# Kernel tuning notes

Hardware: AMD Instinct MI355X
Metric: run time of the kernel (lower is better)

Reference implementation:

```python
import jax, jax.numpy as jnp
from jax import lax
import numpy as np

N = 4
ALPHA_AP = 0.85
ALPHA_DS = 0.1
ALPHA_LR = 1.0
C1 = 0.01 ** 2
C2 = 0.03 ** 2


def resize_ac(img, nh, nw):
    # bilinear resize, align_corners=True (matches F.interpolate(..., align_corners=True))
    B, C, H, W = img.shape
    ys = jnp.linspace(0.0, H - 1.0, nh)
    xs = jnp.linspace(0.0, W - 1.0, nw)
    y0 = jnp.floor(ys).astype(jnp.int32)
    y1 = jnp.minimum(y0 + 1, H - 1)
    x0 = jnp.floor(xs).astype(jnp.int32)
    x1 = jnp.minimum(x0 + 1, W - 1)
    wy = (ys - y0).astype(img.dtype)[None, None, :, None]
    wx = (xs - x0).astype(img.dtype)[None, None, None, :]
    top = img[:, :, y0, :] * (1.0 - wy) + img[:, :, y1, :] * wy
    return top[:, :, :, x0] * (1.0 - wx) + top[:, :, :, x1] * wx


def build_pyramid(img):
    B, C, H, W = img.shape
    pyr = [img]
    for i in range(N - 1):
        r = 2 ** (i + 1)
        pyr.append(resize_ac(pyr[i], H // r, W // r))  # resize previous level, as in torch code
    return pyr


def x_grad(img):
    # replicate-pad right then diff -> last column is exactly zero
    g = img[:, :, :, :-1] - img[:, :, :, 1:]
    return jnp.concatenate([g, jnp.zeros_like(img[:, :, :, :1])], axis=3)


def y_grad(img):
    g = img[:, :, :-1, :] - img[:, :, 1:, :]
    return jnp.concatenate([g, jnp.zeros_like(img[:, :, :1, :])], axis=2)


def avgpool3(x):
    # AvgPool2d(3, 1), VALID padding
    return lax.reduce_window(x, 0.0, lax.add, (1, 1, 3, 3), (1, 1, 1, 1), 'VALID') / 9.0


def grid_sample_zeros(img, gx, gy):
    # bilinear grid_sample, padding_mode='zeros', align_corners=True
    B, C, H, W = img.shape
    x = (gx + 1.0) * 0.5 * (W - 1)
    y = (gy + 1.0) * 0.5 * (H - 1)
    x0 = jnp.floor(x)
    y0 = jnp.floor(y)

    def corner(xi, yi, w):
        valid = (xi >= 0) & (xi <= W - 1) & (yi >= 0) & (yi <= H - 1)
        xc = jnp.clip(xi, 0, W - 1).astype(jnp.int32)
        yc = jnp.clip(yi, 0, H - 1).astype(jnp.int32)
        vals = jax.vmap(lambda im, yy, xx: im[:, yy, xx])(img, yc, xc)  # [B,C,H,W]
        return vals * (w * valid.astype(img.dtype))[:, None]

    return (corner(x0, y0, (x0 + 1 - x) * (y0 + 1 - y))
            + corner(x0 + 1, y0, (x - x0) * (y0 + 1 - y))
            + corner(x0, y0 + 1, (x0 + 1 - x) * (y - y0))
            + corner(x0 + 1, y0 + 1, (x - x0) * (y - y0)))


def apply_disparity(img, disp):
    # standard Monodepth bilinear sampler: shift x_base in [0,1] by disp, grid_sample
    B, C, H, W = img.shape
    x_base = jnp.linspace(0.0, 1.0, W)[None, None, :]
    y_base = jnp.linspace(0.0, 1.0, H)[None, :, None]
    gx = 2.0 * (x_base + disp[:, 0]) - 1.0  # [B,H,W]
    gy = jnp.broadcast_to(2.0 * y_base - 1.0, gx.shape)
    return grid_sample_zeros(img, gx, gy)


def dssim(x, y):
    mu_x = avgpool3(x)
    mu_y = avgpool3(y)
    sig_x = avgpool3(x * x) - mu_x ** 2
    sig_y = avgpool3(y * y) - mu_y ** 2
    cov = avgpool3(x * y) - mu_x * mu_y
    ssim = ((2.0 * mu_x * mu_y + C1) * (2.0 * cov + C2)) / ((mu_x ** 2 + mu_y ** 2 + C1) * (sig_x + sig_y + C2))
    return jnp.mean(jnp.clip((1.0 - ssim) / 2.0, 0.0, 1.0))


def smoothness(disp, img, level):
    wx = jnp.exp(-jnp.mean(jnp.abs(x_grad(img)), axis=1, keepdims=True))
    wy = jnp.exp(-jnp.mean(jnp.abs(y_grad(img)), axis=1, keepdims=True))
    sx = x_grad(disp) * wx
    sy = y_grad(disp) * wy
    return jnp.mean(jnp.abs(sx) + jnp.abs(sy)) / (2 ** level)


def loss_forward(disps, left, right):
    lp = build_pyramid(left)
    rp = build_pyramid(right)
    dl = [d[:, 0:1] for d in disps]
    dr = [d[:, 1:2] for d in disps]
    left_est = [apply_disparity(rp[i], -dl[i]) for i in range(N)]
    right_est = [apply_disparity(lp[i], dr[i]) for i in range(N)]
    r2l_disp = [apply_disparity(dr[i], -dl[i]) for i in range(N)]
    l2r_disp = [apply_disparity(dl[i], dr[i]) for i in range(N)]
    # appearance matching (note: outer *ALPHA_AP matches the original's AP_loss*self.alpha_AP)
    AP = sum(ALPHA_AP * dssim(lp[i], left_est[i]) + (1.0 - ALPHA_AP) * jnp.mean(jnp.abs(lp[i] - left_est[i])) for i in range(N))
    AP = AP + sum(ALPHA_AP * dssim(rp[i], right_est[i]) + (1.0 - ALPHA_AP) * jnp.mean(jnp.abs(rp[i] - right_est[i])) for i in range(N))
    AP = AP * ALPHA_AP
    LR = sum(jnp.mean(jnp.abs(dl[i] - r2l_disp[i])) for i in range(N))
    LR = (LR + sum(jnp.mean(jnp.abs(dr[i] - l2r_disp[i])) for i in range(N))) * ALPHA_LR
    DS = sum(smoothness(dl[i], lp[i], i) for i in range(N))
    DS = (DS + sum(smoothness(dr[i], rp[i], i) for i in range(N))) * ALPHA_DS
    total = AP + LR + DS
    return total, AP, LR, DS


def setup_inputs() -> dict:
    key = jax.random.key(0)
    ks = jax.random.split(key, 6)
    B, H, W = 32, 256, 512
    inp = {}
    for i in range(N):
        h, w = H >> i, W >> i
        # normalized disparities in [0, 0.05) as in trained Monodepth
        inp[f'disp{i}'] = jax.random.uniform(ks[i], (B, 2, h, w), jnp.float32) * 0.05
    inp['left'] = jax.random.uniform(ks[4], (B, 3, H, W), jnp.float32)
    inp['right'] = jax.random.uniform(ks[5], (B, 3, H, W), jnp.float32)
    return inp


def reference(disp0, disp1, disp2, disp3, left, right):
    return loss_forward([disp0, disp1, disp2, disp3], left, right)
```

## Files before the change

### kernel.cpp

```cpp
#include <hip/hip_runtime.h>

#define BDIM 256
#define SH 16

typedef float v2f __attribute__((ext_vector_type(2)));

struct LevelDesc {
    const float* lp; const float* rp; const float* dp;
    int H, W, nCW, nRS, nPerSide, waveBase;
};
struct AllParams { LevelDesc lv[4]; int totalWaves; };

__device__ __forceinline__ float dpp_shl1(float x) {
    int r = __builtin_amdgcn_update_dpp(0, __float_as_int(x), 0x130, 0xF, 0xF, true);
    return __int_as_float(r);
}

__device__ __forceinline__ const float* uptr(const float* p) {
    unsigned long long u = (unsigned long long)p;
    unsigned lo = __builtin_amdgcn_readfirstlane((unsigned)u);
    unsigned hi = __builtin_amdgcn_readfirstlane((unsigned)(u >> 32));
    return (const float*)(((unsigned long long)hi << 32) | (unsigned long long)lo);
}

__device__ __forceinline__ v2f mkv(float a, float b) { v2f r; r.x = a; r.y = b; return r; }


__global__ void resize2_kernel(const float* __restrict__ sL, const float* __restrict__ sR,
                               float* __restrict__ dL, float* __restrict__ dR,
                               int BC, int Hs, int Ws, int Hd, int Wd,
                               double* acc, int doZero) {
    if (doZero && blockIdx.x == 0 && threadIdx.x < 33) acc[threadIdx.x] = 0.0;
    long long half = (long long)BC * Hd * Wd;
    long long idx = (long long)blockIdx.x * blockDim.x + threadIdx.x;
    if (idx >= 2 * half) return;
    const float* src = (idx < half) ? sL : sR;
    float* dst = (idx < half) ? dL : dR;
    long long id = (idx < half) ? idx : idx - half;
    int i = (int)(id % Wd);
    long long t = id / Wd;
    int j = (int)(t % Hd);
    int bc = (int)(t / Hd);
    float stepy = (float)(Hs - 1) / (float)(Hd - 1);
    float stepx = (float)(Ws - 1) / (float)(Wd - 1);
    float y = j * stepy;
    float x = i * stepx;
    int y0 = (int)floorf(y);
    int y1 = min(y0 + 1, Hs - 1);
    int x0 = (int)floorf(x);
    int x1 = min(x0 + 1, Ws - 1);
    float wy = y - (float)y0;
    float wx = x - (float)x0;
    const float* s = src + (long long)bc * Hs * Ws;
    float t0 = s[(long long)y0 * Ws + x0] * (1.0f - wy) + s[(long long)y1 * Ws + x0] * wy;
    float t1 = s[(long long)y0 * Ws + x1] * (1.0f - wy) + s[(long long)y1 * Ws + x1] * wy;
    dst[id] = t0 * (1.0f - wx) + t1 * wx;
}

#define S2Y (127.0f / 63.0f)
#define S2X (255.0f / 127.0f)
#define S3Y (63.0f / 31.0f)
#define S3X (127.0f / 63.0f)

__device__ __forceinline__ float bilA(const float* __restrict__ s, int j, int i) {
    float y = j * S2Y, x = i * S2X;
    int y0 = (int)floorf(y); int y1 = min(y0 + 1, 127);
    int x0 = (int)floorf(x); int x1 = min(x0 + 1, 255);
    float wy = y - (float)y0, wx = x - (float)x0;
    float t0 = s[y0 * 256 + x0] * (1.0f - wy) + s[y1 * 256 + x0] * wy;
    float t1 = s[y0 * 256 + x1] * (1.0f - wy) + s[y1 * 256 + x1] * wy;
    return t0 * (1.0f - wx) + t1 * wx;
}
__device__ __forceinline__ float bilB(const float* __restrict__ s, int j, int i) {
    float y = j * S3Y, x = i * S3X;
    int y0 = (int)floorf(y); int y1 = min(y0 + 1, 63);
    int x0 = (int)floorf(x); int x1 = min(x0 + 1, 127);
    float wy = y - (float)y0, wx = x - (float)x0;
    float v00 = bilA(s, y0, x0), v10 = bilA(s, y1, x0);
    float v01 = bilA(s, y0, x1), v11 = bilA(s, y1, x1);
    float t0 = v00 * (1.0f - wy) + v10 * wy;
    float t1 = v01 * (1.0f - wy) + v11 * wy;
    return t0 * (1.0f - wx) + t1 * wx;
}

__global__ void __launch_bounds__(256)
resize23_kernel(const float* __restrict__ l1, const float* __restrict__ r1,
                float* __restrict__ l2, float* __restrict__ r2,
                float* __restrict__ l3, float* __restrict__ r3) {
    const int n2 = 96 * 64 * 128;
    const int n3 = 96 * 32 * 64;
    int idx = blockIdx.x * 256 + threadIdx.x;
    if (idx < 2 * n2) {
        const float* src = (idx < n2) ? l1 : r1;
        float* dst = (idx < n2) ? l2 : r2;
        int id = (idx < n2) ? idx : idx - n2;
        int i = id & 127, j = (id >> 7) & 63, bc = id >> 13;
        dst[id] = bilA(src + bc * 32768, j, i);
    } else if (idx < 2 * n2 + 2 * n3) {
        int t = idx - 2 * n2;
        const float* src = (t < n3) ? l1 : r1;
        float* dst = (t < n3) ? l3 : r3;
        int id = (t < n3) ? t : t - n3;
        int i = id & 63, j = (id >> 6) & 31, bc = id >> 11;
        dst[id] = bilB(src + bc * 32768, j, i);
    }
}

__device__ __forceinline__ v2f ssim_term2(v2f Sx, v2f Sy, v2f Sxx, v2f Syy, v2f Sxy) {
    const float C1v = 0.0001f;
    const float C2v = 0.0009f;
    const float i9 = 1.0f / 9.0f;
    v2f mux = Sx * i9, muy = Sy * i9;
    v2f sigx = Sxx * i9 - mux * mux;
    v2f sigy = Syy * i9 - muy * muy;
    v2f cov  = Sxy * i9 - mux * muy;
    v2f num = ((2.0f * mux) * muy + C1v) * (2.0f * cov + C2v);
    v2f den = (mux * mux + muy * muy + C1v) * (sigx + sigy + C2v);
    v2f r;
    r.x = __builtin_amdgcn_rcpf(den.x);
    r.y = __builtin_amdgcn_rcpf(den.y);
    v2f v = (1.0f - num * r) * 0.5f;
    v2f o;
    o.x = __builtin_amdgcn_fmed3f(v.x, 0.0f, 1.0f);
    o.y = __builtin_amdgcn_fmed3f(v.y, 0.0f, 1.0f);
    return o;
}

struct RowVals {
    float d0, d1;
    v2f xv[3];
    v2f wI, wJ;
    v2f dI, dJ;
    v2f sI[3], sJ[3];
};

__global__ void __launch_bounds__(BDIM)
mega_kernel(AllParams P, double* __restrict__ acc, float* __restrict__ out) {
    const int lane = threadIdx.x & 63;
    const int wid  = threadIdx.x >> 6;
    const int wId  = blockIdx.x * (BDIM / 64) + wid;
    const int w = min(wId, P.totalWaves - 1);

    int level = 0;
    if (w >= P.lv[1].waveBase) level = 1;
    if (w >= P.lv[2].waveBase) level = 2;
    if (w >= P.lv[3].waveBase) level = 3;
    LevelDesc L;
    if (level == 0) L = P.lv[0];
    else if (level == 1) L = P.lv[1];
    else if (level == 2) L = P.lv[2];
    else L = P.lv[3];

    int rel = w - L.waveBase;
    const int side = (rel >= L.nPerSide) ? 1 : 0;
    rel -= side * L.nPerSide;
    const int cw = rel % L.nCW; rel /= L.nCW;
    const int rs = rel % L.nRS;
    const int b  = rel / L.nRS;

    const int H = L.H, W = L.W;
    const long long HW = (long long)H * W;
    const unsigned HWu = (unsigned)HW;
    const float Wm1f = (float)(W - 1);
    const float sgn = side ? 1.0f : -1.0f;

    const float* xim = uptr((side ? L.rp : L.lp) + (long long)b * 3 * HW);
    const float* sim = uptr((side ? L.lp : L.rp) + (long long)b * 3 * HW);
    const float* dme = uptr(L.dp + (long long)b * 2 * HW + (side ? HW : 0));
    const float* dot = uptr(L.dp + (long long)b * 2 * HW + (side ? 0 : HW));

    const int base = cw * 126;
    const int c0 = base + 2 * lane;
    const int c1 = c0 + 1;
    const bool in0 = c0 < W, in1 = c1 < W;
    const int cc = min(c0, W - 2) >> 1;
    const float fc0 = (float)c0, fc1 = (float)c1;

    const bool lastW = (cw == L.nCW - 1);
    const bool own0 = in0 && (c0 < base + 126 || lastW);
    const bool own1 = in1 && (c1 < base + 126 || lastW);
    const bool ownS0 = own0 && (c0 <= W - 3);
    const bool ownS1 = own1 && (c1 <= W - 3);

    const float mO0 = own0 ? 1.f : 0.f, mO1 = own1 ? 1.f : 0.f;
    const float mS0 = ownS0 ? 1.f : 0.f, mS1 = ownS1 ? 1.f : 0.f;
    const float mX0 = (own0 && c0 < W - 1) ? 1.f : 0.f;
    const float mX1 = (own1 && c1 < W - 1) ? 1.f : 0.f;

    const int r0 = rs * SH;
    const int r1 = min(r0 + SH, H);
    const int jend = min(r1 + 1, H - 1);

    v2f Pst[3][5], Lst[3][5];
#pragma unroll
    for (int c = 0; c < 3; ++c)
#pragma unroll
        for (int s = 0; s < 5; ++s) { Pst[c][s] = mkv(0.f, 0.f); Lst[c][s] = mkv(0.f, 0.f); }
    float pd0 = 0.f, pd1 = 0.f;
    v2f pxv[3] = {mkv(0.f,0.f), mkv(0.f,0.f), mkv(0.f,0.f)};

    float f_ss = 0.f, f_l1 = 0.f, f_lr = 0.f, f_ds = 0.f;

    auto load_dp = [&](int jj, float& o0, float& o1) {
        float2 dpair = ((const float2*)(dme + (unsigned)jj * (unsigned)W))[cc];
        o0 = dpair.x; o1 = dpair.y;
    };

    auto issue_gathers = [&](float di0, float di1, int jj, RowVals& R) {
        const unsigned ro = (unsigned)jj * (unsigned)W;
        R.d0 = di0; R.d1 = di1;
        float xq0 = fmaf(sgn * di0, Wm1f, fc0);
        float xq1 = fmaf(sgn * di1, Wm1f, fc1);
        float xf0 = floorf(xq0), xf1 = floorf(xq1);
        int g0 = (int)xf0, g1 = (int)xf1;
        float t0 = xq0 - xf0, t1 = xq1 - xf1;
        float w00 = (in0 && g0 >= 0 && g0 < W)         ? 1.0f - t0 : 0.0f;
        float w01 = (in0 && g0 >= -1 && g0 < W - 1)    ? t0        : 0.0f;
        float w10 = (in1 && g1 >= 0 && g1 < W)         ? 1.0f - t1 : 0.0f;
        float w11 = (in1 && g1 >= -1 && g1 < W - 1)    ? t1        : 0.0f;
        R.wI = mkv(w00, w10);
        R.wJ = mkv(w01, w11);
        unsigned a0 = ro + (unsigned)min(max(g0, 0), W - 1);
        unsigned a1 = ro + (unsigned)min(max(g0 + 1, 0), W - 1);
        unsigned b0 = ro + (unsigned)min(max(g1, 0), W - 1);
        unsigned b1 = ro + (unsigned)min(max(g1 + 1, 0), W - 1);
        R.dI = mkv(dot[a0], dot[b0]);
        R.dJ = mkv(dot[a1], dot[b1]);
#pragma unroll
        for (int c = 0; c < 3; ++c) {
            const unsigned co = (unsigned)c * HWu;
            float2 xp2 = ((const float2*)(xim + co + ro))[cc];
            R.xv[c] = mkv(in0 ? xp2.x : 0.f, in1 ? xp2.y : 0.f);
            R.sI[c] = mkv(sim[co + a0], sim[co + b0]);
            R.sJ[c] = mkv(sim[co + a1], sim[co + b1]);
        }
    };

    auto consume = [&](const RowVals& R, int j) {
        const float d0 = R.d0, d1 = R.d1;
        v2f wv2 = R.dI * R.wI + R.dJ * R.wJ;
        v2f xv[3], yv[3];
#pragma unroll
        for (int c = 0; c < 3; ++c) {
            xv[c] = R.xv[c];
            yv[c] = R.sI[c] * R.wI + R.sJ[c] * R.wJ;
        }

        const bool rowOwn = j < r1;
        if (rowOwn) {
            float s0 = fabsf(xv[0].x - yv[0].x) + fabsf(xv[1].x - yv[1].x) + fabsf(xv[2].x - yv[2].x);
            float s1 = fabsf(xv[0].y - yv[0].y) + fabsf(xv[1].y - yv[1].y) + fabsf(xv[2].y - yv[2].y);
            f_l1 = fmaf(mO0, s0, f_l1);
            f_l1 = fmaf(mO1, s1, f_l1);
            f_lr = fmaf(mO0, fabsf(d0 - wv2.x), f_lr);
            f_lr = fmaf(mO1, fabsf(d1 - wv2.y), f_lr);
        }

        {
            float dn  = dpp_shl1(d0);
            float xn0 = dpp_shl1(xv[0].x);
            float xn1 = dpp_shl1(xv[1].x);
            float xn2 = dpp_shl1(xv[2].x);
            if (rowOwn) {
                float g0v = fabsf(xv[0].x - xv[0].y) + fabsf(xv[1].x - xv[1].y) + fabsf(xv[2].x - xv[2].y);
                float g1v = fabsf(xv[0].y - xn0) + fabsf(xv[1].y - xn1) + fabsf(xv[2].y - xn2);
                f_ds = fmaf(mX0, fabsf((d0 - d1) * __expf(-g0v * (1.0f / 3.0f))), f_ds);
                f_ds = fmaf(mX1, fabsf((d1 - dn) * __expf(-g1v * (1.0f / 3.0f))), f_ds);
            }
        }
        if (j > r0 && (j - 1) < r1) {
            v2f t0 = pxv[0] - xv[0];
            v2f t1 = pxv[1] - xv[1];
            v2f t2 = pxv[2] - xv[2];
            float g0v = fabsf(t0.x) + fabsf(t1.x) + fabsf(t2.x);
            float g1v = fabsf(t0.y) + fabsf(t1.y) + fabsf(t2.y);
            f_ds = fmaf(mO0, fabsf((pd0 - d0) * __expf(-g0v * (1.0f / 3.0f))), f_ds);
            f_ds = fmaf(mO1, fabsf((pd1 - d1) * __expf(-g1v * (1.0f / 3.0f))), f_ds);
        }
        pd0 = d0; pd1 = d1;
#pragma unroll
        for (int c = 0; c < 3; ++c) pxv[c] = xv[c];

        const bool emit = (j >= r0 + 2);
#pragma unroll
        for (int c = 0; c < 3; ++c) {
            v2f X = xv[c], Y = yv[c];
            v2f V[5];
            V[0] = X; V[1] = Y;
            V[2] = X * X; V[3] = Y * Y; V[4] = X * Y;
            v2f cs[5];
#pragma unroll
            for (int s = 0; s < 5; ++s) {
                cs[s] = Pst[c][s] + V[s];
                Pst[c][s] = Lst[c][s] + V[s];
                Lst[c][s] = V[s];
            }
            if (emit) {
                v2f Wn[5];
#pragma unroll
                for (int s = 0; s < 5; ++s) {
                    float s0 = cs[s].x + cs[s].y;
                    Wn[s].x = s0 + dpp_shl1(cs[s].x);
                    Wn[s].y = cs[s].y + dpp_shl1(s0);
                }
                v2f ts = ssim_term2(Wn[0], Wn[1], Wn[2], Wn[3], Wn[4]);
                f_ss = fmaf(mS0, ts.x, f_ss);
                f_ss = fmaf(mS1, ts.y, f_ss);
            }
        }
    };

    RowVals A, B;
    float dq0, dq1, dn0, dn1;
    load_dp(r0, dq0, dq1);
    load_dp(min(r0 + 1, jend), dn0, dn1);
    issue_gathers(dq0, dq1, r0, A);

    int j = r0;
    for (;;) {
        float dp20, dp21;
        load_dp(min(j + 2, jend), dp20, dp21);
        if (j < jend) issue_gathers(dn0, dn1, j + 1, B);
        consume(A, j);
        dn0 = dp20; dn1 = dp21;
        if (++j > jend) break;

        load_dp(min(j + 2, jend), dp20, dp21);
        if (j < jend) issue_gathers(dn0, dn1, j + 1, A);
        consume(B, j);
        dn0 = dp20; dn1 = dp21;
        if (++j > jend) break;
    }

#pragma unroll
    for (int o = 32; o > 0; o >>= 1) {
        f_ss += __shfl_down(f_ss, o);
        f_l1 += __shfl_down(f_l1, o);
        f_lr += __shfl_down(f_lr, o);
        f_ds += __shfl_down(f_ds, o);
    }
    __shared__ float red[BDIM / 64][4];
    __shared__ int meta[2];
    if (threadIdx.x == 0) { meta[0] = level; meta[1] = side; }
    if (lane == 0) {
        red[wid][0] = f_ss; red[wid][1] = f_l1;
        red[wid][2] = f_lr; red[wid][3] = f_ds;
    }
    __syncthreads();
    if (threadIdx.x < 4) {
        int t = threadIdx.x;
        double s = (double)red[0][t] + (double)red[1][t]
                 + (double)red[2][t] + (double)red[3][t];
        atomicAdd(acc + t * 8 + meta[1] * 4 + meta[0], s);
    }

    if (threadIdx.x == 0) {
        asm volatile("s_waitcnt vmcnt(0)" ::: "memory");
        unsigned old = atomicAdd((unsigned*)(acc + 32), 1u);
        if (old == (unsigned)(gridDim.x - 1)) {
            const int B_ = 32, H0 = 256, W0 = 512;
            double AP = 0.0, LR = 0.0, DS = 0.0;
            for (int i = 0; i < 4; ++i) {
                int h = H0 >> i, ww = W0 >> i;
                double nss = (double)B_ * 3.0 * (double)(h - 2) * (double)(ww - 2);
                double nl1 = (double)B_ * 3.0 * (double)h * (double)ww;
                double nd  = (double)B_ * (double)h * (double)ww;
                double a0  = atomicAdd(acc + 0  + i, 0.0);
                double a4  = atomicAdd(acc + 4  + i, 0.0);
                double a8  = atomicAdd(acc + 8  + i, 0.0);
                double a12 = atomicAdd(acc + 12 + i, 0.0);
                double a16 = atomicAdd(acc + 16 + i, 0.0);
                double a20 = atomicAdd(acc + 20 + i, 0.0);
                double a24 = atomicAdd(acc + 24 + i, 0.0);
                double a28 = atomicAdd(acc + 28 + i, 0.0);
                AP += 0.85 * (a0 / nss) + 0.15 * (a8 / nl1);
                AP += 0.85 * (a4 / nss) + 0.15 * (a12 / nl1);
                LR += a16 / nd + a20 / nd;
                double sc = 1.0 / (double)(1 << i);
                DS += (a24 / nd) * sc + (a28 / nd) * sc;
            }
            AP *= 0.85;
            DS *= 0.1;
            double total = AP + LR + DS;
            out[0] = (float)total;
            out[1] = (float)AP;
            out[2] = (float)LR;
            out[3] = (float)DS;
        }
    }
}

extern "C" void kernel_launch(void* const* d_in, const int* in_sizes, int n_in,
                              void* d_out, int out_size, void* d_ws, size_t ws_size,
                              hipStream_t stream) {
    const int B = 32, H0 = 256, W0 = 512;
    const float* dsp[4];
    for (int i = 0; i < 4; ++i) dsp[i] = (const float*)d_in[i];
    const float* left  = (const float*)d_in[4];
    const float* right = (const float*)d_in[5];
    float* out = (float*)d_out;

    double* acc = (double*)d_ws;
    float* buf = (float*)((char*)d_ws + 512);

    const float* lp[4];
    const float* rp[4];
    float* lpm[4];
    float* rpm[4];
    lp[0] = left; rp[0] = right;
    float* cur = buf;
    for (int i = 1; i < 4; ++i) { lpm[i] = cur; cur += (long long)B * 3 * (H0 >> i) * (W0 >> i); }
    for (int i = 1; i < 4; ++i) { rpm[i] = cur; cur += (long long)B * 3 * (H0 >> i) * (W0 >> i); }
    for (int i = 1; i < 4; ++i) { lp[i] = lpm[i]; rp[i] = rpm[i]; }

    {
        long long half = (long long)B * 3 * 128 * 256;
        int g = (int)((2 * half + BDIM - 1) / BDIM);
        resize2_kernel<<<g, BDIM, 0, stream>>>(
            lp[0], rp[0], lpm[1], rpm[1], B * 3, 256, 512, 128, 256, acc, 1);
    }
    {
        int n2 = 96 * 64 * 128, n3 = 96 * 32 * 64;
        int total = 2 * (n2 + n3);
        int g = (total + 255) / 256;
        resize23_kernel<<<g, 256, 0, stream>>>(lpm[1], rpm[1], lpm[2], rpm[2],
                                               lpm[3], rpm[3]);
    }

    AllParams P;
    int wb = 0;
    for (int i = 0; i < 4; ++i) {
        int h = H0 >> i, w = W0 >> i;
        LevelDesc& L = P.lv[i];
        L.lp = lp[i]; L.rp = rp[i]; L.dp = dsp[i];
        L.H = h; L.W = w;
        L.nCW = (w - 2 + 125) / 126;
        L.nRS = h / SH;
        L.nPerSide = B * L.nRS * L.nCW;
        L.waveBase = wb;
        wb += 2 * L.nPerSide;
    }
    P.totalWaves = wb;
    int blocks = (wb + (BDIM / 64) - 1) / (BDIM / 64);
    mega_kernel<<<blocks, BDIM, 0, stream>>>(P, acc, out);
}
```

Measured before the change: 293.2 us.

## Fuse resize and loss passes into one persistent cooperative kernel with grid syncs

Replaces the three launches (two resize kernels and the loss mega kernel) with a single cooperative persistent kernel. The kernel uses grid-stride loops and grid.sync() between the pyramid stages, and loops waves over the tiles. Per-wave results now go straight to global atomics instead of a block-level LDS reduction, and the final scalar combine runs after a last grid sync rather than through a ticket counter. This saves launch overhead and inter-kernel gaps, at the cost of grid-wide barrier latency, occupancy capped at the cooperative grid size, and more global atomic traffic.

```diff
diff --git a/kernel.cpp b/kernel.cpp
--- a/kernel.cpp
+++ b/kernel.cpp
@@ -1,4 +1,7 @@
 #include <hip/hip_runtime.h>
+#include <hip/hip_cooperative_groups.h>
+
+namespace cg = cooperative_groups;
 
 #define BDIM 256
 #define SH 16
@@ -10,6 +13,12 @@
     int H, W, nCW, nRS, nPerSide, waveBase;
 };
 struct AllParams { LevelDesc lv[4]; int totalWaves; };
+struct FArgs {
+    AllParams P;
+    const float* left; const float* right;
+    float *l1, *r1, *l2, *r2, *l3, *r3;
+    double* acc; float* out;
+};
 
 __device__ __forceinline__ float dpp_shl1(float x) {
     int r = __builtin_amdgcn_update_dpp(0, __float_as_int(x), 0x130, 0xF, 0xF, true);
@@ -25,43 +34,22 @@
 
 __device__ __forceinline__ v2f mkv(float a, float b) { v2f r; r.x = a; r.y = b; return r; }
 
-
-__global__ void resize2_kernel(const float* __restrict__ sL, const float* __restrict__ sR,
-                               float* __restrict__ dL, float* __restrict__ dR,
-                               int BC, int Hs, int Ws, int Hd, int Wd,
-                               double* acc, int doZero) {
-    if (doZero && blockIdx.x == 0 && threadIdx.x < 33) acc[threadIdx.x] = 0.0;
-    long long half = (long long)BC * Hd * Wd;
-    long long idx = (long long)blockIdx.x * blockDim.x + threadIdx.x;
-    if (idx >= 2 * half) return;
-    const float* src = (idx < half) ? sL : sR;
-    float* dst = (idx < half) ? dL : dR;
-    long long id = (idx < half) ? idx : idx - half;
-    int i = (int)(id % Wd);
-    long long t = id / Wd;
-    int j = (int)(t % Hd);
-    int bc = (int)(t / Hd);
-    float stepy = (float)(Hs - 1) / (float)(Hd - 1);
-    float stepx = (float)(Ws - 1) / (float)(Wd - 1);
-    float y = j * stepy;
-    float x = i * stepx;
-    int y0 = (int)floorf(y);
-    int y1 = min(y0 + 1, Hs - 1);
-    int x0 = (int)floorf(x);
-    int x1 = min(x0 + 1, Ws - 1);
-    float wy = y - (float)y0;
-    float wx = x - (float)x0;
-    const float* s = src + (long long)bc * Hs * Ws;
-    float t0 = s[(long long)y0 * Ws + x0] * (1.0f - wy) + s[(long long)y1 * Ws + x0] * wy;
-    float t1 = s[(long long)y0 * Ws + x1] * (1.0f - wy) + s[(long long)y1 * Ws + x1] * wy;
-    dst[id] = t0 * (1.0f - wx) + t1 * wx;
-}
-
+#define S1Y (255.0f / 127.0f)
+#define S1X (511.0f / 255.0f)
 #define S2Y (127.0f / 63.0f)
 #define S2X (255.0f / 127.0f)
 #define S3Y (63.0f / 31.0f)
 #define S3X (127.0f / 63.0f)
 
+__device__ __forceinline__ float bil0(const float* __restrict__ s, int j, int i) {
+    float y = j * S1Y, x = i * S1X;
+    int y0 = (int)floorf(y); int y1 = min(y0 + 1, 255);
+    int x0 = (int)floorf(x); int x1 = min(x0 + 1, 511);
+    float wy = y - (float)y0, wx = x - (float)x0;
+    float t0 = s[y0 * 512 + x0] * (1.0f - wy) + s[y1 * 512 + x0] * wy;
+    float t1 = s[y0 * 512 + x1] * (1.0f - wy) + s[y1 * 512 + x1] * wy;
+    return t0 * (1.0f - wx) + t1 * wx;
+}
 __device__ __forceinline__ float bilA(const float* __restrict__ s, int j, int i) {
     float y = j * S2Y, x = i * S2X;
     int y0 = (int)floorf(y); int y1 = min(y0 + 1, 127);
@@ -81,29 +69,6 @@
     float t0 = v00 * (1.0f - wy) + v10 * wy;
     float t1 = v01 * (1.0f - wy) + v11 * wy;
     return t0 * (1.0f - wx) + t1 * wx;
-}
-
-__global__ void __launch_bounds__(256)
-resize23_kernel(const float* __restrict__ l1, const float* __restrict__ r1,
-                float* __restrict__ l2, float* __restrict__ r2,
-                float* __restrict__ l3, float* __restrict__ r3) {
-    const int n2 = 96 * 64 * 128;
-    const int n3 = 96 * 32 * 64;
-    int idx = blockIdx.x * 256 + threadIdx.x;
-    if (idx < 2 * n2) {
-        const float* src = (idx < n2) ? l1 : r1;
-        float* dst = (idx < n2) ? l2 : r2;
-        int id = (idx < n2) ? idx : idx - n2;
-        int i = id & 127, j = (id >> 7) & 63, bc = id >> 13;
-        dst[id] = bilA(src + bc * 32768, j, i);
-    } else if (idx < 2 * n2 + 2 * n3) {
-        int t = idx - 2 * n2;
-        const float* src = (t < n3) ? l1 : r1;
-        float* dst = (t < n3) ? l3 : r3;
-        int id = (t < n3) ? t : t - n3;
-        int i = id & 63, j = (id >> 6) & 31, bc = id >> 11;
-        dst[id] = bilB(src + bc * 32768, j, i);
-    }
 }
 
 __device__ __forceinline__ v2f ssim_term2(v2f Sx, v2f Sy, v2f Sxx, v2f Syy, v2f Sxy) {
@@ -134,259 +99,290 @@
     v2f sI[3], sJ[3];
 };
 
-__global__ void __launch_bounds__(BDIM)
-mega_kernel(AllParams P, double* __restrict__ acc, float* __restrict__ out) {
+__global__ void __launch_bounds__(BDIM, 4)
+fused_kernel(FArgs K) {
+    cg::grid_group grid = cg::this_grid();
+    const int tid = blockIdx.x * BDIM + (int)threadIdx.x;
+    const int nth = gridDim.x * BDIM;
+
+    if (tid < 32) atomicExch((unsigned long long*)(K.acc + tid), 0ull);
+
+    {
+        const int n1 = 96 * 128 * 256;
+        for (int idx = tid; idx < 2 * n1; idx += nth) {
+            const float* src = (idx < n1) ? K.left : K.right;
+            float* dst = (idx < n1) ? K.l1 : K.r1;
+            int id = (idx < n1) ? idx : idx - n1;
+            int i = id & 255, j = (id >> 8) & 127, bc = id >> 15;
+            dst[id] = bil0(src + bc * 131072, j, i);
+        }
+    }
+    grid.sync();
+
+    {
+        const int n2 = 96 * 64 * 128;
+        const int n3 = 96 * 32 * 64;
+        for (int idx = tid; idx < 2 * (n2 + n3); idx += nth) {
+            if (idx < 2 * n2) {
+                const float* src = (idx < n2) ? K.l1 : K.r1;
+                float* dst = (idx < n2) ? K.l2 : K.r2;
+                int id = (idx < n2) ? idx : idx - n2;
+                int i = id & 127, j = (id >> 7) & 63, bc = id >> 13;
+                dst[id] = bilA(src + bc * 32768, j, i);
+            } else {
+                int t = idx - 2 * n2;
+                const float* src = (t < n3) ? K.l1 : K.r1;
+                float* dst = (t < n3) ? K.l3 : K.r3;
+                int id = (t < n3) ? t : t - n3;
+                int i = id & 63, j = (id >> 6) & 31, bc = id >> 11;
+                dst[id] = bilB(src + bc * 32768, j, i);
+            }
+        }
+    }
+    grid.sync();
+
     const int lane = threadIdx.x & 63;
-    const int wid  = threadIdx.x >> 6;
-    const int wId  = blockIdx.x * (BDIM / 64) + wid;
-    const int w = min(wId, P.totalWaves - 1);
-
-    int level = 0;
-    if (w >= P.lv[1].waveBase) level = 1;
-    if (w >= P.lv[2].waveBase) level = 2;
-    if (w >= P.lv[3].waveBase) level = 3;
-    LevelDesc L;
-    if (level == 0) L = P.lv[0];
-    else if (level == 1) L = P.lv[1];
-    else if (level == 2) L = P.lv[2];
-    else L = P.lv[3];
-
-    int rel = w - L.waveBase;
-    const int side = (rel >= L.nPerSide) ? 1 : 0;
-    rel -= side * L.nPerSide;
-    const int cw = rel % L.nCW; rel /= L.nCW;
-    const int rs = rel % L.nRS;
-    const int b  = rel / L.nRS;
-
-    const int H = L.H, W = L.W;
-    const long long HW = (long long)H * W;
-    const unsigned HWu = (unsigned)HW;
-    const float Wm1f = (float)(W - 1);
-    const float sgn = side ? 1.0f : -1.0f;
-
-    const float* xim = uptr((side ? L.rp : L.lp) + (long long)b * 3 * HW);
-    const float* sim = uptr((side ? L.lp : L.rp) + (long long)b * 3 * HW);
-    const float* dme = uptr(L.dp + (long long)b * 2 * HW + (side ? HW : 0));
-    const float* dot = uptr(L.dp + (long long)b * 2 * HW + (side ? 0 : HW));
-
-    const int base = cw * 126;
-    const int c0 = base + 2 * lane;
-    const int c1 = c0 + 1;
-    const bool in0 = c0 < W, in1 = c1 < W;
-    const int cc = min(c0, W - 2) >> 1;
-    const float fc0 = (float)c0, fc1 = (float)c1;
-
-    const bool lastW = (cw == L.nCW - 1);
-    const bool own0 = in0 && (c0 < base + 126 || lastW);
-    const bool own1 = in1 && (c1 < base + 126 || lastW);
-    const bool ownS0 = own0 && (c0 <= W - 3);
-    const bool ownS1 = own1 && (c1 <= W - 3);
-
-    const float mO0 = own0 ? 1.f : 0.f, mO1 = own1 ? 1.f : 0.f;
-    const float mS0 = ownS0 ? 1.f : 0.f, mS1 = ownS1 ? 1.f : 0.f;
-    const float mX0 = (own0 && c0 < W - 1) ? 1.f : 0.f;
-    const float mX1 = (own1 && c1 < W - 1) ? 1.f : 0.f;
-
-    const int r0 = rs * SH;
-    const int r1 = min(r0 + SH, H);
-    const int jend = min(r1 + 1, H - 1);
-
-    v2f Pst[3][5], Lst[3][5];
-#pragma unroll
-    for (int c = 0; c < 3; ++c)
-#pragma unroll
-        for (int s = 0; s < 5; ++s) { Pst[c][s] = mkv(0.f, 0.f); Lst[c][s] = mkv(0.f, 0.f); }
-    float pd0 = 0.f, pd1 = 0.f;
-    v2f pxv[3] = {mkv(0.f,0.f), mkv(0.f,0.f), mkv(0.f,0.f)};
-
-    float f_ss = 0.f, f_l1 = 0.f, f_lr = 0.f, f_ds = 0.f;
-
-    auto load_dp = [&](int jj, float& o0, float& o1) {
-        float2 dpair = ((const float2*)(dme + (unsigned)jj * (unsigned)W))[cc];
-        o0 = dpair.x; o1 = dpair.y;
-    };
-
-    auto issue_gathers = [&](float di0, float di1, int jj, RowVals& R) {
-        const unsigned ro = (unsigned)jj * (unsigned)W;
-        R.d0 = di0; R.d1 = di1;
-        float xq0 = fmaf(sgn * di0, Wm1f, fc0);
-        float xq1 = fmaf(sgn * di1, Wm1f, fc1);
-        float xf0 = floorf(xq0), xf1 = floorf(xq1);
-        int g0 = (int)xf0, g1 = (int)xf1;
-        float t0 = xq0 - xf0, t1 = xq1 - xf1;
-        float w00 = (in0 && g0 >= 0 && g0 < W)         ? 1.0f - t0 : 0.0f;
-        float w01 = (in0 && g0 >= -1 && g0 < W - 1)    ? t0        : 0.0f;
-        float w10 = (in1 && g1 >= 0 && g1 < W)         ? 1.0f - t1 : 0.0f;
-        float w11 = (in1 && g1 >= -1 && g1 < W - 1)    ? t1        : 0.0f;
-        R.wI = mkv(w00, w10);
-        R.wJ = mkv(w01, w11);
-        unsigned a0 = ro + (unsigned)min(max(g0, 0), W - 1);
-        unsigned a1 = ro + (unsigned)min(max(g0 + 1, 0), W - 1);
-        unsigned b0 = ro + (unsigned)min(max(g1, 0), W - 1);
-        unsigned b1 = ro + (unsigned)min(max(g1 + 1, 0), W - 1);
-        R.dI = mkv(dot[a0], dot[b0]);
-        R.dJ = mkv(dot[a1], dot[b1]);
-#pragma unroll
-        for (int c = 0; c < 3; ++c) {
-            const unsigned co = (unsigned)c * HWu;
-            float2 xp2 = ((const float2*)(xim + co + ro))[cc];
-            R.xv[c] = mkv(in0 ? xp2.x : 0.f, in1 ? xp2.y : 0.f);
-            R.sI[c] = mkv(sim[co + a0], sim[co + b0]);
-            R.sJ[c] = mkv(sim[co + a1], sim[co + b1]);
-        }
-    };
-
-    auto consume = [&](const RowVals& R, int j) {
-        const float d0 = R.d0, d1 = R.d1;
-        v2f wv2 = R.dI * R.wI + R.dJ * R.wJ;
-        v2f xv[3], yv[3];
-#pragma unroll
-        for (int c = 0; c < 3; ++c) {
-            xv[c] = R.xv[c];
-            yv[c] = R.sI[c] * R.wI + R.sJ[c] * R.wJ;
-        }
-
-        const bool rowOwn = j < r1;
-        if (rowOwn) {
-            float s0 = fabsf(xv[0].x - yv[0].x) + fabsf(xv[1].x - yv[1].x) + fabsf(xv[2].x - yv[2].x);
-            float s1 = fabsf(xv[0].y - yv[0].y) + fabsf(xv[1].y - yv[1].y) + fabsf(xv[2].y - yv[2].y);
-            f_l1 = fmaf(mO0, s0, f_l1);
-            f_l1 = fmaf(mO1, s1, f_l1);
-            f_lr = fmaf(mO0, fabsf(d0 - wv2.x), f_lr);
-            f_lr = fmaf(mO1, fabsf(d1 - wv2.y), f_lr);
-        }
-
-        {
-            float dn  = dpp_shl1(d0);
-            float xn0 = dpp_shl1(xv[0].x);
-            float xn1 = dpp_shl1(xv[1].x);
-            float xn2 = dpp_shl1(xv[2].x);
+    const int gw = blockIdx.x * (BDIM / 64) + ((int)threadIdx.x >> 6);
+    const int gwN = gridDim.x * (BDIM / 64);
+
+    for (int w = gw; w < K.P.totalWaves; w += gwN) {
+        int level = 0;
+        if (w >= K.P.lv[1].waveBase) level = 1;
+        if (w >= K.P.lv[2].waveBase) level = 2;
+        if (w >= K.P.lv[3].waveBase) level = 3;
+        LevelDesc L;
+        if (level == 0) L = K.P.lv[0];
+        else if (level == 1) L = K.P.lv[1];
+        else if (level == 2) L = K.P.lv[2];
+        else L = K.P.lv[3];
+
+        int rel = w - L.waveBase;
+        const int side = (rel >= L.nPerSide) ? 1 : 0;
+        rel -= side * L.nPerSide;
+        const int cw = rel % L.nCW; rel /= L.nCW;
+        const int rs = rel % L.nRS;
+        const int b  = rel / L.nRS;
+
+        const int H = L.H, W = L.W;
+        const long long HW = (long long)H * W;
+        const unsigned HWu = (unsigned)HW;
+        const float Wm1f = (float)(W - 1);
+        const float sgn = side ? 1.0f : -1.0f;
+
+        const float* xim = uptr((side ? L.rp : L.lp) + (long long)b * 3 * HW);
+        const float* sim = uptr((side ? L.lp : L.rp) + (long long)b * 3 * HW);
+        const float* dme = uptr(L.dp + (long long)b * 2 * HW + (side ? HW : 0));
+        const float* dot = uptr(L.dp + (long long)b * 2 * HW + (side ? 0 : HW));
+
+        const int base = cw * 126;
+        const int c0 = base + 2 * lane;
+        const int c1 = c0 + 1;
+        const bool in0 = c0 < W, in1 = c1 < W;
+        const int cc = min(c0, W - 2) >> 1;
+        const float fc0 = (float)c0, fc1 = (float)c1;
+
+        const bool lastW = (cw == L.nCW - 1);
+        const bool own0 = in0 && (c0 < base + 126 || lastW);
+        const bool own1 = in1 && (c1 < base + 126 || lastW);
+        const bool ownS0 = own0 && (c0 <= W - 3);
+        const bool ownS1 = own1 && (c1 <= W - 3);
+
+        const float mO0 = own0 ? 1.f : 0.f, mO1 = own1 ? 1.f : 0.f;
+        const float mS0 = ownS0 ? 1.f : 0.f, mS1 = ownS1 ? 1.f : 0.f;
+        const float mX0 = (own0 && c0 < W - 1) ? 1.f : 0.f;
+        const float mX1 = (own1 && c1 < W - 1) ? 1.f : 0.f;
+
+        const int r0 = rs * SH;
+        const int r1 = min(r0 + SH, H);
+        const int jend = min(r1 + 1, H - 1);
+
+        v2f Pst[3][5], Lst[3][5];
+#pragma unroll
+        for (int c = 0; c < 3; ++c)
+#pragma unroll
+            for (int s = 0; s < 5; ++s) { Pst[c][s] = mkv(0.f, 0.f); Lst[c][s] = mkv(0.f, 0.f); }
+        float pd0 = 0.f, pd1 = 0.f;
+        v2f pxv[3] = {mkv(0.f,0.f), mkv(0.f,0.f), mkv(0.f,0.f)};
+
+        float f_ss = 0.f, f_l1 = 0.f, f_lr = 0.f, f_ds = 0.f;
+
+        auto load_dp = [&](int jj, float& o0, float& o1) {
+            float2 dpair = ((const float2*)(dme + (unsigned)jj * (unsigned)W))[cc];
+            o0 = dpair.x; o1 = dpair.y;
+        };
+
+        auto issue_gathers = [&](float di0, float di1, int jj, RowVals& R) {
+            const unsigned ro = (unsigned)jj * (unsigned)W;
+            R.d0 = di0; R.d1 = di1;
+            float xq0 = fmaf(sgn * di0, Wm1f, fc0);
+            float xq1 = fmaf(sgn * di1, Wm1f, fc1);
+            float xf0 = floorf(xq0), xf1 = floorf(xq1);
+            int g0 = (int)xf0, g1 = (int)xf1;
+            float t0 = xq0 - xf0, t1 = xq1 - xf1;
+            float w00 = (in0 && g0 >= 0 && g0 < W)         ? 1.0f - t0 : 0.0f;
+            float w01 = (in0 && g0 >= -1 && g0 < W - 1)    ? t0        : 0.0f;
+            float w10 = (in1 && g1 >= 0 && g1 < W)         ? 1.0f - t1 : 0.0f;
+            float w11 = (in1 && g1 >= -1 && g1 < W - 1)    ? t1        : 0.0f;
+            R.wI = mkv(w00, w10);
+            R.wJ = mkv(w01, w11);
+            unsigned a0 = ro + (unsigned)min(max(g0, 0), W - 1);
+            unsigned a1 = ro + (unsigned)min(max(g0 + 1, 0), W - 1);
+            unsigned b0 = ro + (unsigned)min(max(g1, 0), W - 1);
+            unsigned b1 = ro + (unsigned)min(max(g1 + 1, 0), W - 1);
+            R.dI = mkv(dot[a0], dot[b0]);
+            R.dJ = mkv(dot[a1], dot[b1]);
+#pragma unroll
+            for (int c = 0; c < 3; ++c) {
+                const unsigned co = (unsigned)c * HWu;
+                float2 xp2 = ((const float2*)(xim + co + ro))[cc];
+                R.xv[c] = mkv(in0 ? xp2.x : 0.f, in1 ? xp2.y : 0.f);
+                R.sI[c] = mkv(sim[co + a0], sim[co + b0]);
+                R.sJ[c] = mkv(sim[co + a1], sim[co + b1]);
+            }
+        };
+
+        auto consume = [&](const RowVals& R, int j) {
+            const float d0 = R.d0, d1 = R.d1;
+            v2f wv2 = R.dI * R.wI + R.dJ * R.wJ;
+            v2f xv[3], yv[3];
+#pragma unroll
+            for (int c = 0; c < 3; ++c) {
+                xv[c] = R.xv[c];
+                yv[c] = R.sI[c] * R.wI + R.sJ[c] * R.wJ;
+            }
+
+            const bool rowOwn = j < r1;
             if (rowOwn) {
-                float g0v = fabsf(xv[0].x - xv[0].y) + fabsf(xv[1].x - xv[1].y) + fabsf(xv[2].x - xv[2].y);
-                float g1v = fabsf(xv[0].y - xn0) + fabsf(xv[1].y - xn1) + fabsf(xv[2].y - xn2);
-                f_ds = fmaf(mX0, fabsf((d0 - d1) * __expf(-g0v * (1.0f / 3.0f))), f_ds);
-                f_ds = fmaf(mX1, fabsf((d1 - dn) * __expf(-g1v * (1.0f / 3.0f))), f_ds);
-            }
-        }
-        if (j > r0 && (j - 1) < r1) {
-            v2f t0 = pxv[0] - xv[0];
-            v2f t1 = pxv[1] - xv[1];
-            v2f t2 = pxv[2] - xv[2];
-            float g0v = fabsf(t0.x) + fabsf(t1.x) + fabsf(t2.x);
-            float g1v = fabsf(t0.y) + fabsf(t1.y) + fabsf(t2.y);
-            f_ds = fmaf(mO0, fabsf((pd0 - d0) * __expf(-g0v * (1.0f / 3.0f))), f_ds);
-            f_ds = fmaf(mO1, fabsf((pd1 - d1) * __expf(-g1v * (1.0f / 3.0f))), f_ds);
-        }
-        pd0 = d0; pd1 = d1;
-#pragma unroll
-        for (int c = 0; c < 3; ++c) pxv[c] = xv[c];
-
-        const bool emit = (j >= r0 + 2);
-#pragma unroll
-        for (int c = 0; c < 3; ++c) {
-            v2f X = xv[c], Y = yv[c];
-            v2f V[5];
-            V[0] = X; V[1] = Y;
-            V[2] = X * X; V[3] = Y * Y; V[4] = X * Y;
-            v2f cs[5];
-#pragma unroll
-            for (int s = 0; s < 5; ++s) {
-                cs[s] = Pst[c][s] + V[s];
-                Pst[c][s] = Lst[c][s] + V[s];
-                Lst[c][s] = V[s];
-            }
-            if (emit) {
-                v2f Wn[5];
+                float s0 = fabsf(xv[0].x - yv[0].x) + fabsf(xv[1].x - yv[1].x) + fabsf(xv[2].x - yv[2].x);
+                float s1 = fabsf(xv[0].y - yv[0].y) + fabsf(xv[1].y - yv[1].y) + fabsf(xv[2].y - yv[2].y);
+                f_l1 = fmaf(mO0, s0, f_l1);
+                f_l1 = fmaf(mO1, s1, f_l1);
+                f_lr = fmaf(mO0, fabsf(d0 - wv2.x), f_lr);
+                f_lr = fmaf(mO1, fabsf(d1 - wv2.y), f_lr);
+            }
+
+            {
+                float dn  = dpp_shl1(d0);
+                float xn0 = dpp_shl1(xv[0].x);
+                float xn1 = dpp_shl1(xv[1].x);
+                float xn2 = dpp_shl1(xv[2].x);
+                if (rowOwn) {
+                    float g0v = fabsf(xv[0].x - xv[0].y) + fabsf(xv[1].x - xv[1].y) + fabsf(xv[2].x - xv[2].y);
+                    float g1v = fabsf(xv[0].y - xn0) + fabsf(xv[1].y - xn1) + fabsf(xv[2].y - xn2);
+                    f_ds = fmaf(mX0, fabsf((d0 - d1) * __expf(-g0v * (1.0f / 3.0f))), f_ds);
+                    f_ds = fmaf(mX1, fabsf((d1 - dn) * __expf(-g1v * (1.0f / 3.0f))), f_ds);
+                }
+            }
+            if (j > r0 && (j - 1) < r1) {
+                v2f t0 = pxv[0] - xv[0];
+                v2f t1 = pxv[1] - xv[1];
+                v2f t2 = pxv[2] - xv[2];
+                float g0v = fabsf(t0.x) + fabsf(t1.x) + fabsf(t2.x);
+                float g1v = fabsf(t0.y) + fabsf(t1.y) + fabsf(t2.y);
+                f_ds = fmaf(mO0, fabsf((pd0 - d0) * __expf(-g0v * (1.0f / 3.0f))), f_ds);
+                f_ds = fmaf(mO1, fabsf((pd1 - d1) * __expf(-g1v * (1.0f / 3.0f))), f_ds);
+            }
+            pd0 = d0; pd1 = d1;
+#pragma unroll
+            for (int c = 0; c < 3; ++c) pxv[c] = xv[c];
+
+            const bool emit = (j >= r0 + 2);
+#pragma unroll
+            for (int c = 0; c < 3; ++c) {
+                v2f X = xv[c], Y = yv[c];
+                v2f V[5];
+                V[0] = X; V[1] = Y;
+                V[2] = X * X; V[3] = Y * Y; V[4] = X * Y;
+                v2f cs[5];
 #pragma unroll
                 for (int s = 0; s < 5; ++s) {
-                    float s0 = cs[s].x + cs[s].y;
-                    Wn[s].x = s0 + dpp_shl1(cs[s].x);
-                    Wn[s].y = cs[s].y + dpp_shl1(s0);
+                    cs[s] = Pst[c][s] + V[s];
+                    Pst[c][s] = Lst[c][s] + V[s];
+                    Lst[c][s] = V[s];
                 }
-                v2f ts = ssim_term2(Wn[0], Wn[1], Wn[2], Wn[3], Wn[4]);
-                f_ss = fmaf(mS0, ts.x, f_ss);
-                f_ss = fmaf(mS1, ts.y, f_ss);
-            }
-        }
-    };
-
-    RowVals A, B;
-    float dq0, dq1, dn0, dn1;
-    load_dp(r0, dq0, dq1);
-    load_dp(min(r0 + 1, jend), dn0, dn1);
-    issue_gathers(dq0, dq1, r0, A);
-
-    int j = r0;
-    for (;;) {
-        float dp20, dp21;
-        load_dp(min(j + 2, jend), dp20, dp21);
-        if (j < jend) issue_gathers(dn0, dn1, j + 1, B);
-        consume(A, j);
-        dn0 = dp20; dn1 = dp21;
-        if (++j > jend) break;
-
-        load_dp(min(j + 2, jend), dp20, dp21);
-        if (j < jend) issue_gathers(dn0, dn1, j + 1, A);
-        consume(B, j);
-        dn0 = dp20; dn1 = dp21;
-        if (++j > jend) break;
-    }
-
-#pragma unroll
-    for (int o = 32; o > 0; o >>= 1) {
-        f_ss += __shfl_down(f_ss, o);
-        f_l1 += __shfl_down(f_l1, o);
-        f_lr += __shfl_down(f_lr, o);
-        f_ds += __shfl_down(f_ds, o);
-    }
-    __shared__ float red[BDIM / 64][4];
-    __shared__ int meta[2];
-    if (threadIdx.x == 0) { meta[0] = level; meta[1] = side; }
-    if (lane == 0) {
-        red[wid][0] = f_ss; red[wid][1] = f_l1;
-        red[wid][2] = f_lr; red[wid][3] = f_ds;
-    }
-    __syncthreads();
-    if (threadIdx.x < 4) {
-        int t = threadIdx.x;
-        double s = (double)red[0][t] + (double)red[1][t]
-                 + (double)red[2][t] + (double)red[3][t];
-        atomicAdd(acc + t * 8 + meta[1] * 4 + meta[0], s);
-    }
-
-    if (threadIdx.x == 0) {
-        asm volatile("s_waitcnt vmcnt(0)" ::: "memory");
-        unsigned old = atomicAdd((unsigned*)(acc + 32), 1u);
-        if (old == (unsigned)(gridDim.x - 1)) {
-            const int B_ = 32, H0 = 256, W0 = 512;
-            double AP = 0.0, LR = 0.0, DS = 0.0;
-            for (int i = 0; i < 4; ++i) {
-                int h = H0 >> i, ww = W0 >> i;
-                double nss = (double)B_ * 3.0 * (double)(h - 2) * (double)(ww - 2);
-                double nl1 = (double)B_ * 3.0 * (double)h * (double)ww;
-                double nd  = (double)B_ * (double)h * (double)ww;
-                double a0  = atomicAdd(acc + 0  + i, 0.0);
-                double a4  = atomicAdd(acc + 4  + i, 0.0);
-                double a8  = atomicAdd(acc + 8  + i, 0.0);
-                double a12 = atomicAdd(acc + 12 + i, 0.0);
-                double a16 = atomicAdd(acc + 16 + i, 0.0);
-                double a20 = atomicAdd(acc + 20 + i, 0.0);
-                double a24 = atomicAdd(acc + 24 + i, 0.0);
-                double a28 = atomicAdd(acc + 28 + i, 0.0);
-                AP += 0.85 * (a0 / nss) + 0.15 * (a8 / nl1);
-                AP += 0.85 * (a4 / nss) + 0.15 * (a12 / nl1);
-                LR += a16 / nd + a20 / nd;
-                double sc = 1.0 / (double)(1 << i);
-                DS += (a24 / nd) * sc + (a28 / nd) * sc;
-            }
-            AP *= 0.85;
-            DS *= 0.1;
-            double total = AP + LR + DS;
-            out[0] = (float)total;
-            out[1] = (float)AP;
-            out[2] = (float)LR;
-            out[3] = (float)DS;
-        }
+                if (emit) {
+                    v2f Wn[5];
+#pragma unroll
+                    for (int s = 0; s < 5; ++s) {
+                        float s0 = cs[s].x + cs[s].y;
+                        Wn[s].x = s0 + dpp_shl1(cs[s].x);
+                        Wn[s].y = cs[s].y + dpp_shl1(s0);
+                    }
+                    v2f ts = ssim_term2(Wn[0], Wn[1], Wn[2], Wn[3], Wn[4]);
+                    f_ss = fmaf(mS0, ts.x, f_ss);
+                    f_ss = fmaf(mS1, ts.y, f_ss);
+                }
+            }
+        };
+
+        RowVals RA, RB;
+        float dq0, dq1, dn0, dn1;
+        load_dp(r0, dq0, dq1);
+        load_dp(min(r0 + 1, jend), dn0, dn1);
+        issue_gathers(dq0, dq1, r0, RA);
+
+        int j = r0;
+        for (;;) {
+            float dp20, dp21;
+            load_dp(min(j + 2, jend), dp20, dp21);
+            if (j < jend) issue_gathers(dn0, dn1, j + 1, RB);
+            consume(RA, j);
+            dn0 = dp20; dn1 = dp21;
+            if (++j > jend) break;
+
+            load_dp(min(j + 2, jend), dp20, dp21);
+            if (j < jend) issue_gathers(dn0, dn1, j + 1, RA);
+            consume(RB, j);
+            dn0 = dp20; dn1 = dp21;
+            if (++j > jend) break;
+        }
+
+#pragma unroll
+        for (int o = 32; o > 0; o >>= 1) {
+            f_ss += __shfl_down(f_ss, o);
+            f_l1 += __shfl_down(f_l1, o);
+            f_lr += __shfl_down(f_lr, o);
+            f_ds += __shfl_down(f_ds, o);
+        }
+        if (lane == 0) {
+            atomicAdd(K.acc + 0  + side * 4 + level, (double)f_ss);
+            atomicAdd(K.acc + 8  + side * 4 + level, (double)f_l1);
+            atomicAdd(K.acc + 16 + side * 4 + level, (double)f_lr);
+            atomicAdd(K.acc + 24 + side * 4 + level, (double)f_ds);
+        }
+    }
+    grid.sync();
+
+    if (tid == 0) {
+        double* acc = K.acc;
+        const int B_ = 32, H0 = 256, W0 = 512;
+        double AP = 0.0, LR = 0.0, DS = 0.0;
+        for (int i = 0; i < 4; ++i) {
+            int h = H0 >> i, ww = W0 >> i;
+            double nss = (double)B_ * 3.0 * (double)(h - 2) * (double)(ww - 2);
+            double nl1 = (double)B_ * 3.0 * (double)h * (double)ww;
+            double nd  = (double)B_ * (double)h * (double)ww;
+            double a0  = atomicAdd(acc + 0  + i, 0.0);
+            double a4  = atomicAdd(acc + 4  + i, 0.0);
+            double a8  = atomicAdd(acc + 8  + i, 0.0);
+            double a12 = atomicAdd(acc + 12 + i, 0.0);
+            double a16 = atomicAdd(acc + 16 + i, 0.0);
+            double a20 = atomicAdd(acc + 20 + i, 0.0);
+            double a24 = atomicAdd(acc + 24 + i, 0.0);
+            double a28 = atomicAdd(acc + 28 + i, 0.0);
+            AP += 0.85 * (a0 / nss) + 0.15 * (a8 / nl1);
+            AP += 0.85 * (a4 / nss) + 0.15 * (a12 / nl1);
+            LR += a16 / nd + a20 / nd;
+            double sc = 1.0 / (double)(1 << i);
+            DS += (a24 / nd) * sc + (a28 / nd) * sc;
+        }
+        AP *= 0.85;
+        DS *= 0.1;
+        double total = AP + LR + DS;
+        K.out[0] = (float)total;
+        K.out[1] = (float)AP;
+        K.out[2] = (float)LR;
+        K.out[3] = (float)DS;
     }
 }
 
@@ -413,25 +409,11 @@
     for (int i = 1; i < 4; ++i) { rpm[i] = cur; cur += (long long)B * 3 * (H0 >> i) * (W0 >> i); }
     for (int i = 1; i < 4; ++i) { lp[i] = lpm[i]; rp[i] = rpm[i]; }
 
-    {
-        long long half = (long long)B * 3 * 128 * 256;
-        int g = (int)((2 * half + BDIM - 1) / BDIM);
-        resize2_kernel<<<g, BDIM, 0, stream>>>(
-            lp[0], rp[0], lpm[1], rpm[1], B * 3, 256, 512, 128, 256, acc, 1);
-    }
-    {
-        int n2 = 96 * 64 * 128, n3 = 96 * 32 * 64;
-        int total = 2 * (n2 + n3);
-        int g = (total + 255) / 256;
-        resize23_kernel<<<g, 256, 0, stream>>>(lpm[1], rpm[1], lpm[2], rpm[2],
-                                               lpm[3], rpm[3]);
-    }
-
-    AllParams P;
+    FArgs K;
     int wb = 0;
     for (int i = 0; i < 4; ++i) {
         int h = H0 >> i, w = W0 >> i;
-        LevelDesc& L = P.lv[i];
+        LevelDesc& L = K.P.lv[i];
         L.lp = lp[i]; L.rp = rp[i]; L.dp = dsp[i];
         L.H = h; L.W = w;
         L.nCW = (w - 2 + 125) / 126;
@@ -440,7 +422,24 @@
         L.waveBase = wb;
         wb += 2 * L.nPerSide;
     }
-    P.totalWaves = wb;
-    int blocks = (wb + (BDIM / 64) - 1) / (BDIM / 64);
-    mega_kernel<<<blocks, BDIM, 0, stream>>>(P, acc, out);
-}
+    K.P.totalWaves = wb;
+    K.left = left; K.right = right;
+    K.l1 = lpm[1]; K.r1 = rpm[1];
+    K.l2 = lpm[2]; K.r2 = rpm[2];
+    K.l3 = lpm[3]; K.r3 = rpm[3];
+    K.acc = acc; K.out = out;
+
+    static int s_grid = 0;
+    if (s_grid == 0) {
+        int perCU = 0;
+        if (hipOccupancyMaxActiveBlocksPerMultiprocessor(&perCU, fused_kernel, BDIM, 0)
+                != hipSuccess || perCU < 1)
+            perCU = 4;
+        s_grid = perCU * 256;
+        int maxUseful = (wb + (BDIM / 64) - 1) / (BDIM / 64);
+        if (s_grid > maxUseful) s_grid = maxUseful;
+    }
+
+    void* ka[] = { (void*)&K };
+    hipLaunchCooperativeKernel(fused_kernel, dim3(s_grid), dim3(BDIM), ka, 0, stream);
+}
```

Result: slower. 981.7 us (+234.8%).
